# Optimization experiments

Hardware: AMD Instinct MI355X
Metric: run time of the kernel (lower is better)

## Reference

```python
import jax, jax.numpy as jnp
import numpy as np

EPS = 1e-5  # BatchNorm eps (torch default)

def _bn(x, gamma, beta):
    # training-mode BatchNorm over the edge/node (leading) axis, biased var
    mean = x.mean(axis=0, keepdims=True)
    var = x.var(axis=0, keepdims=True)
    return (x - mean) * jax.lax.rsqrt(var + EPS) * gamma + beta

def _silu(x):
    return x * jax.nn.sigmoid(x)

def setup_inputs() -> dict:
    N, E, H, NH = 50000, 800000, 128, 4
    HD = H // NH
    key = jax.random.key(0)
    ks = jax.random.split(key, 8)
    x = jax.random.normal(ks[0], (N, H), dtype=jnp.float32)
    weight = jax.random.uniform(ks[1], (N, 1), dtype=jnp.float32)  # positive fraction weights
    src = jax.random.randint(ks[2], (E,), 0, N)
    dst = jax.random.randint(ks[3], (E,), 0, N)
    # f: Linear(2H, 1) + BN(1)
    Wf = jax.random.normal(ks[4], (2 * H, 1), dtype=jnp.float32) * 0.05
    bf = jnp.zeros((1,), jnp.float32)
    f_gamma = jnp.ones((1,), jnp.float32)
    f_beta = jnp.zeros((1,), jnp.float32)
    # g: NH heads of Linear(2H, HD) + BN(HD), stacked on leading head axis
    Wg = jax.random.normal(ks[5], (NH, 2 * H, HD), dtype=jnp.float32) * 0.05
    bg = jnp.zeros((NH, HD), jnp.float32)
    g_gamma = jnp.ones((NH, HD), jnp.float32)
    g_beta = jnp.zeros((NH, HD), jnp.float32)
    # bn_nodes: BN(H)
    n_gamma = jnp.ones((H,), jnp.float32)
    n_beta = jnp.zeros((H,), jnp.float32)
    return dict(x=x, weight=weight, src=src, dst=dst, Wf=Wf, bf=bf,
                f_gamma=f_gamma, f_beta=f_beta, Wg=Wg, bg=bg,
                g_gamma=g_gamma, g_beta=g_beta, n_gamma=n_gamma, n_beta=n_beta)

def reference(x, weight, src, dst, Wf, bf, f_gamma, f_beta, Wg, bg, g_gamma, g_beta, n_gamma, n_beta):
    N = x.shape[0]
    E = src.shape[0]
    # per-edge concat of src/dst node features: [E, 2H]
    hihj = jnp.concatenate([x[src], x[dst]], axis=-1)
    # attention logit f(hihj) = SiLU(BN(Linear)) then exp: [E, 1]
    exp_e = jnp.exp(_silu(_bn(hihj @ Wf + bf, f_gamma, f_beta)))
    # weighted softmax-like normalization over incoming edges of each dst node
    we = weight[src] * exp_e                                   # [E, 1]
    sum_w_exp = jax.ops.segment_sum(we, dst, num_segments=N)   # [N, 1]
    a = we / sum_w_exp[dst]                                    # [E, 1]
    # multi-head message: a_ij * SiLU(BN(Linear_h(hihj))) per head, concat
    z = jnp.einsum('ed,hdk->ehk', hihj, Wg) + bg               # [E, NH, HD]
    z = _silu(_bn(z, g_gamma, g_beta))
    msg = (a[:, :, None] * z).reshape(E, -1)                   # [E, H]
    h = jax.ops.segment_sum(msg, dst, num_segments=N)          # [N, H]
    out = _bn(h, n_gamma, n_beta) + x                          # residual
    return out
```

## Files before the change

kernel.cpp:

```cpp
#include <hip/hip_runtime.h>
#include <hip/hip_bf16.h>
#include <math.h>

#define HDIM 128
#define PAD 64
#define QCAP 8192
typedef unsigned short ushort_t;
typedef unsigned int uint_t;
typedef __attribute__((ext_vector_type(8))) short bf16x8;
typedef __attribute__((ext_vector_type(4))) float f32x4;
typedef __attribute__((ext_vector_type(2))) float v2f;

__device__ __forceinline__ float wave_allreduce(float v){
  #pragma unroll
  for (int o = 1; o < 64; o <<= 1) v += __shfl_xor(v, o);
  return v;
}

__device__ __forceinline__ ushort_t f2bf(float f){
  uint_t u = __float_as_uint(f);
  uint_t r = (u + 0x7fffu + ((u >> 16) & 1u)) >> 16;
  return (ushort_t)r;
}

__device__ __forceinline__ v2f bf2(uint_t u){
  v2f r;
  r.x = __uint_as_float(u << 16);
  r.y = __uint_as_float(u & 0xffff0000u);
  return r;
}

__global__ __launch_bounds__(256) void k_wpack(const float* __restrict__ Wg,
    const float* __restrict__ Wf, ushort_t* __restrict__ W3,
    const int* __restrict__ src, const int* __restrict__ dst,
    uint_t* __restrict__ queue, int* __restrict__ tails, int E){
  int b = blockIdx.x;
  if (b < 272){
    int k = threadIdx.x;
    if (k >= 128) return;
    float val;
    if (b < 128)       val = Wg[(size_t)(b >> 5) * 8192 + k * 32 + (b & 31)];
    else if (b < 256){ int c2 = b - 128;
                       val = Wg[(size_t)(c2 >> 5) * 8192 + (k + 128) * 32 + (c2 & 31)]; }
    else if (b == 256) val = Wf[k];
    else if (b == 257) val = Wf[128 + k];
    else               val = 0.f;
    int idx = (((b >> 4) * 4 + (k >> 5)) * 16 + (b & 15)) * 32 + (k & 31);
    W3[idx] = f2bf(val);
    return;
  }
  __shared__ int hist[256], gbase[256];
  int t = threadIdx.x;
  hist[t] = 0;
  __syncthreads();
  int e0 = ((b - 272) * 256 + t) * 8;
  int d0=0,d1=0,d2=0,d3=0,d4=0,d5=0,d6=0,d7=0;
  int s0=0,s1=0,s2=0,s3=0,s4=0,s5=0,s6=0,s7=0;
  bool v0=e0<E, v1=e0+1<E, v2=e0+2<E, v3=e0+3<E,
       v4=e0+4<E, v5=e0+5<E, v6=e0+6<E, v7=e0+7<E;
  if (v7 && (e0 + 8 <= E)){
    int4 da = *(const int4*)(dst + e0); int4 db_ = *(const int4*)(dst + e0 + 4);
    int4 sa = *(const int4*)(src + e0); int4 sb_ = *(const int4*)(src + e0 + 4);
    d0=da.x; d1=da.y; d2=da.z; d3=da.w; d4=db_.x; d5=db_.y; d6=db_.z; d7=db_.w;
    s0=sa.x; s1=sa.y; s2=sa.z; s3=sa.w; s4=sb_.x; s5=sb_.y; s6=sb_.z; s7=sb_.w;
  } else {
    if (v0){ d0=dst[e0];   s0=src[e0];   }
    if (v1){ d1=dst[e0+1]; s1=src[e0+1]; }
    if (v2){ d2=dst[e0+2]; s2=src[e0+2]; }
    if (v3){ d3=dst[e0+3]; s3=src[e0+3]; }
    if (v4){ d4=dst[e0+4]; s4=src[e0+4]; }
    if (v5){ d5=dst[e0+5]; s5=src[e0+5]; }
    if (v6){ d6=dst[e0+6]; s6=src[e0+6]; }
    if (v7){ d7=dst[e0+7]; s7=src[e0+7]; }
  }
#define DIST1(i) int b##i = d##i >> 8, r##i = 0; \
    if (v##i) r##i = atomicAdd(&hist[b##i], 1);
  DIST1(0) DIST1(1) DIST1(2) DIST1(3) DIST1(4) DIST1(5) DIST1(6) DIST1(7)
#undef DIST1
  __syncthreads();
  if (hist[t]) gbase[t] = atomicAdd(&tails[t], hist[t]);
  __syncthreads();
#define DISTW(i) if (v##i){ int q = gbase[b##i] + r##i; if (q < QCAP) \
    queue[(size_t)b##i * QCAP + q] = ((uint_t)(d##i & 255) << 16) | (uint_t)s##i; }
  DISTW(0) DISTW(1) DISTW(2) DISTW(3) DISTW(4) DISTW(5) DISTW(6) DISTW(7)
#undef DISTW
}

__global__ __launch_bounds__(256) void k_gemmfill(const float* __restrict__ x,
    const ushort_t* __restrict__ W3, const float* __restrict__ weight,
    ushort_t* __restrict__ Pb, ushort_t* __restrict__ Qb,
    float* __restrict__ v, float2* __restrict__ uw2,
    const uint_t* __restrict__ queue, const int* __restrict__ tails,
    int* __restrict__ cnt, int* __restrict__ es,
    int N, int BK){
  __shared__ ushort_t smem[16384];
  __shared__ int lcnt[256];
  int tid = threadIdx.x;
  if ((int)blockIdx.x < BK){
    int b = blockIdx.x;
    lcnt[tid] = 0;
    __syncthreads();
    int count = tails[b]; if (count > QCAP) count = QCAP;
    for (int i = tid; i < count; i += 256){
      uint_t pk = queue[(size_t)b * QCAP + i];
      int dl = pk >> 16;
      int slot = atomicAdd(&lcnt[dl], 1);
      if (slot < PAD) smem[dl * 64 + slot] = (ushort_t)(pk & 0xffffu);
    }
    __syncthreads();
    int nb = b << 8;
    for (int i = tid; i < 16384; i += 256){
      int n = nb + (i >> 6);
      if (n < N) es[(size_t)nb * 64 + i] = (int)smem[i];
    }
    int n = nb + tid;
    if (n < N){ int c = lcnt[tid]; cnt[n] = c < PAD ? c : PAD; }
  } else {
    ushort_t* xl = smem;
    ushort_t* cl = smem + 4096;
    int n_base = ((int)blockIdx.x - BK) * 32;
    #pragma unroll
    for (int i = 0; i < 4; ++i){
      int cidx = i * 256 + tid;
      int row = cidx >> 5, ch = cidx & 31;
      int rowc = n_base + row; rowc = rowc < N ? rowc : N - 1;
      float4 a = *(const float4*)(x + (size_t)rowc * HDIM + ch * 4);
      uint_t lo = (uint_t)f2bf(a.x) | ((uint_t)f2bf(a.y) << 16);
      uint_t hi = (uint_t)f2bf(a.z) | ((uint_t)f2bf(a.w) << 16);
      int bo = (row * 256 + ch * 8) ^ ((row & 7) << 4);
      *(uint2*)((char*)xl + bo) = make_uint2(lo, hi);
    }
    __syncthreads();
    int wid = __builtin_amdgcn_readfirstlane(tid >> 6);
    int lane = tid & 63;
    int quad = lane >> 4, col = lane & 15;
    int strip = wid >> 1;
    int half = wid & 1;
    int tbeg = half * 8;
    int ntile = half ? 9 : 8;
    f32x4 acc[9];
    #pragma unroll
    for (int t = 0; t < 9; ++t) acc[t] = (f32x4){0.f, 0.f, 0.f, 0.f};
    int arow = strip * 16 + col;
    #pragma unroll
    for (int kk = 0; kk < 4; ++kk){
      int abyte = (arow * 256 + kk * 64 + quad * 16) ^ ((col & 7) << 4);
      bf16x8 af = *(const bf16x8*)((char*)xl + abyte);
      const ushort_t* wb = W3 + (size_t)(tbeg * 4 + kk) * 512 + col * 32 + quad * 8;
      #pragma unroll
      for (int t = 0; t < 9; ++t){
        if (t < ntile){
          bf16x8 bfr = *(const bf16x8*)(wb + (size_t)t * 2048);
          acc[t] = __builtin_amdgcn_mfma_f32_16x16x32_bf16(af, bfr, acc[t], 0, 0, 0);
        }
      }
    }
    #pragma unroll
    for (int t = 0; t < 8; ++t){
      int ct = tbeg + t;
      #pragma unroll
      for (int r = 0; r < 4; ++r){
        int lr = strip * 16 + quad * 4 + r;
        cl[lr * 264 + ct * 16 + col] = f2bf(acc[t][r]);
      }
    }
    if (half){
      #pragma unroll
      for (int r = 0; r < 4; ++r){
        int n = n_base + strip * 16 + quad * 4 + r;
        if (n < N){
          float val = acc[8][r];
          if (col == 0)      uw2[n] = make_float2(val, weight[n]);
          else if (col == 1) v[n] = val;
        }
      }
    }
    __syncthreads();
    int row = tid >> 3, seg = tid & 7;
    int n = n_base + row;
    if (n < N){
      const ushort_t* s = cl + row * 264 + seg * 32;
      uint4 w0 = *(const uint4*)(s);
      uint4 w1 = *(const uint4*)(s + 8);
      uint4 w2 = *(const uint4*)(s + 16);
      uint4 w3v = *(const uint4*)(s + 24);
      if (seg < 4){
        ushort_t* dp = Pb + (size_t)n * HDIM + seg * 32;
        *(uint4*)(dp) = w0; *(uint4*)(dp + 8) = w1;
        *(uint4*)(dp + 16) = w2; *(uint4*)(dp + 24) = w3v;
      } else {
        ushort_t* dp = Qb + (size_t)n * HDIM + (seg - 4) * 32;
        *(uint4*)(dp) = w0; *(uint4*)(dp + 8) = w1;
        *(uint4*)(dp + 16) = w2; *(uint4*)(dp + 24) = w3v;
      }
    }
  }
}

#define SH8(sjv,jj,S) \
  int S##0=__shfl(sjv,(jj)),   S##1=__shfl(sjv,(jj)+1), S##2=__shfl(sjv,(jj)+2), S##3=__shfl(sjv,(jj)+3), \
      S##4=__shfl(sjv,(jj)+4), S##5=__shfl(sjv,(jj)+5), S##6=__shfl(sjv,(jj)+6), S##7=__shfl(sjv,(jj)+7);
#define LD8(S,P) \
  uint_t P##0=Pu[(size_t)S##0*64+lane], P##1=Pu[(size_t)S##1*64+lane], \
         P##2=Pu[(size_t)S##2*64+lane], P##3=Pu[(size_t)S##3*64+lane], \
         P##4=Pu[(size_t)S##4*64+lane], P##5=Pu[(size_t)S##5*64+lane], \
         P##6=Pu[(size_t)S##6*64+lane], P##7=Pu[(size_t)S##7*64+lane];
#define SH4(sjv,jj,S) \
  int S##0=__shfl(sjv,(jj)),   S##1=__shfl(sjv,(jj)+1), S##2=__shfl(sjv,(jj)+2), S##3=__shfl(sjv,(jj)+3);
#define LD4(S,P) \
  uint_t P##0=Pu[(size_t)S##0*64+lane], P##1=Pu[(size_t)S##1*64+lane], \
         P##2=Pu[(size_t)S##2*64+lane], P##3=Pu[(size_t)S##3*64+lane];

__global__ __launch_bounds__(256) void k_gstats(const ushort_t* __restrict__ Pb,
    const ushort_t* __restrict__ Qb, const float* __restrict__ v,
    const float2* __restrict__ uw2, const int* __restrict__ es,
    const int* __restrict__ cnt, float* __restrict__ pstatG, int N){
  int lane = threadIdx.x & 63;
  int wid = __builtin_amdgcn_readfirstlane(threadIdx.x >> 6);
  int part = (int)blockIdx.x & 7;
  int Npp = (N + 7) >> 3;
  int lo = part * Npp;
  int hi = lo + Npp; if (hi > N) hi = N;
  int stp = (gridDim.x >> 3) << 2;
  const uint_t* Pu = (const uint_t*)Pb;
  const uint_t* Qu = (const uint_t*)Qb;
  v2f gs = {0.f,0.f}, gq = {0.f,0.f};
  float fs = 0.f, fq = 0.f;
  int n0 = lo + ((blockIdx.x >> 3) << 2) + wid;
  int n1 = n0 + stp;
  int dnA=0,sjA=0; uint_t qAu=0; float vA=0.f;
  int dnB=0,sjB=0; uint_t qBu=0; float vB=0.f;
  if (n0 < hi){ dnA=cnt[n0]; sjA=es[(size_t)n0*PAD+lane];
                qAu=Qu[(size_t)n0*64+lane]; vA=v[n0]; }
  if (n1 < hi){ dnB=cnt[n1]; sjB=es[(size_t)n1*PAD+lane];
                qBu=Qu[(size_t)n1*64+lane]; vB=v[n1]; }
#define GST(p,Sv,Qv) { v2f y=bf2(p); Sv+=y; Qv.x=fmaf(y.x,y.x,Qv.x); Qv.y=fmaf(y.y,y.y,Qv.y); }
#define GED8(P,Sv,Qv) GST(P##0,Sv,Qv) GST(P##1,Sv,Qv) GST(P##2,Sv,Qv) GST(P##3,Sv,Qv) \
                      GST(P##4,Sv,Qv) GST(P##5,Sv,Qv) GST(P##6,Sv,Qv) GST(P##7,Sv,Qv)
#define GED4(P,Sv,Qv) GST(P##0,Sv,Qv) GST(P##1,Sv,Qv) GST(P##2,Sv,Qv) GST(P##3,Sv,Qv)
  while (n0 < hi){
    int m0 = n0 + 2*stp, m1 = n1 + 2*stp;
    int dnC=0,sjC=0; uint_t qCu=0; float vC=0.f;
    int dnD=0,sjD=0; uint_t qDu=0; float vD=0.f;
    if (m0 < hi){ dnC=cnt[m0]; sjC=es[(size_t)m0*PAD+lane];
                  qCu=Qu[(size_t)m0*64+lane]; vC=v[m0]; }
    if (m1 < hi){ dnD=cnt[m1]; sjD=es[(size_t)m1*PAD+lane];
                  qDu=Qu[(size_t)m1*64+lane]; vD=v[m1]; }
    int dA = dnA < PAD ? dnA : PAD;
    int dB = (n1 < hi) ? (dnB < PAD ? dnB : PAD) : 0;
    if (lane < dA){ float2 uw = uw2[sjA]; float t = uw.x + vA; fs += t; fq = fmaf(t,t,fq); }
    if (lane < dB){ float2 uw = uw2[sjB]; float t = uw.x + vB; fs += t; fq = fmaf(t,t,fq); }
    v2f qa = bf2(qAu), qb = bf2(qBu);
    v2f SnA={0.f,0.f}, SSA={0.f,0.f}, SnB={0.f,0.f}, SSB={0.f,0.f};
    int j0 = 0, j1 = 0;
    for (; j0 + 7 < dA && j1 + 7 < dB; j0 += 8, j1 += 8){
      SH8(sjA,j0,xa) SH8(sjB,j1,xb)
      LD8(xa,pa) LD8(xb,pb)
      GED8(pa,SnA,SSA) GED8(pb,SnB,SSB)
    }
    for (; j0 + 7 < dA; j0 += 8){ SH8(sjA,j0,xa) LD8(xa,pa) GED8(pa,SnA,SSA) }
    for (; j0 + 3 < dA; j0 += 4){ SH4(sjA,j0,xa) LD4(xa,pa) GED4(pa,SnA,SSA) }
    for (; j0 < dA; ++j0){ int s0=__shfl(sjA,j0); uint_t p0=Pu[(size_t)s0*64+lane]; GST(p0,SnA,SSA) }
    for (; j1 + 7 < dB; j1 += 8){ SH8(sjB,j1,xb) LD8(xb,pb) GED8(pb,SnB,SSB) }
    for (; j1 + 3 < dB; j1 += 4){ SH4(sjB,j1,xb) LD4(xb,pb) GED4(pb,SnB,SSB) }
    for (; j1 < dB; ++j1){ int s0=__shfl(sjB,j1); uint_t p0=Pu[(size_t)s0*64+lane]; GST(p0,SnB,SSB) }
    float dAf = (float)dA, dBf = (float)dB;
    gs.x += SnA.x + SnB.x + dAf*qa.x + dBf*qb.x;
    gs.y += SnA.y + SnB.y + dAf*qa.y + dBf*qb.y;
    gq.x += SSA.x + SSB.x + qa.x*fmaf(dAf,qa.x,2.f*SnA.x) + qb.x*fmaf(dBf,qb.x,2.f*SnB.x);
    gq.y += SSA.y + SSB.y + qa.y*fmaf(dAf,qa.y,2.f*SnA.y) + qb.y*fmaf(dBf,qb.y,2.f*SnB.y);
    n0 = m0; n1 = m1;
    dnA=dnC; sjA=sjC; qAu=qCu; vA=vC;
    dnB=dnD; sjB=sjD; qBu=qDu; vB=vD;
  }
#undef GST
#undef GED8
#undef GED4
  fs = wave_allreduce(fs); fq = wave_allreduce(fq);
  __shared__ float red[4][258];
  red[wid][2*lane]       = gs.x; red[wid][2*lane+1]   = gs.y;
  red[wid][128+2*lane]   = gq.x; red[wid][129+2*lane] = gq.y;
  if (lane == 0){ red[wid][256] = fs; red[wid][257] = fq; }
  __syncthreads();
  for (int c = threadIdx.x; c < 258; c += 256)
    pstatG[(size_t)blockIdx.x * 258 + c] = red[0][c] + red[1][c] + red[2][c] + red[3][c];
}

__global__ __launch_bounds__(256) void k_redfin1(const float* __restrict__ pstatG,
    int NB, const float* __restrict__ g_gamma, const float* __restrict__ g_beta,
    const float* __restrict__ f_gamma, const float* __restrict__ f_beta,
    float* __restrict__ fin, long long E){
  int j = blockIdx.x;
  int c1 = (j < 128) ? j : 256;
  int c2 = (j < 128) ? 128 + j : 257;
  double s1 = 0, s2 = 0;
  for (int b = threadIdx.x; b < NB; b += 256){
    const float* pb = pstatG + (size_t)b * 258;
    s1 += (double)pb[c1]; s2 += (double)pb[c2];
  }
  __shared__ double m1[256], m2[256];
  m1[threadIdx.x] = s1; m2[threadIdx.x] = s2;
  __syncthreads();
  for (int o = 128; o; o >>= 1){
    if (threadIdx.x < o){ m1[threadIdx.x] += m1[threadIdx.x + o];
                          m2[threadIdx.x] += m2[threadIdx.x + o]; }
    __syncthreads();
  }
  if (threadIdx.x == 0){
    double m = m1[0] / (double)E;
    double var = m2[0] / (double)E - m * m;
    if (j < 128){
      float sc = (float)((double)g_gamma[j] / sqrt(var + 1e-5));
      fin[2 + j] = sc; fin[130 + j] = g_beta[j] - (float)m * sc;
    } else {
      float sc = (float)((double)f_gamma[0] / sqrt(var + 1e-5));
      fin[0] = sc; fin[1] = f_beta[0] - (float)m * sc;
    }
  }
}

__global__ __launch_bounds__(256) void k_msg(const ushort_t* __restrict__ Pb,
    const ushort_t* __restrict__ Qb, const float* __restrict__ v,
    const float2* __restrict__ uw2, const int* __restrict__ es,
    const int* __restrict__ cnt, const float* __restrict__ fin,
    float* __restrict__ h, float* __restrict__ pstatH, int N){
  int lane = threadIdx.x & 63;
  int wid = __builtin_amdgcn_readfirstlane(threadIdx.x >> 6);
  int part = (int)blockIdx.x & 7;
  int Npp = (N + 7) >> 3;
  int lo = part * Npp;
  int hi = lo + Npp; if (hi > N) hi = N;
  int stp = (gridDim.x >> 3) << 2;
  const uint_t* Pu = (const uint_t*)Pb;
  const uint_t* Qu = (const uint_t*)Qb;
  float fsc = fin[0], fsh = fin[1];
  v2f gsc = {fin[2 + 2*lane], fin[3 + 2*lane]};
  v2f gsh = {fin[130 + 2*lane], fin[131 + 2*lane]};
  v2f hs = {0.f,0.f}, hq = {0.f,0.f};
  int n0 = lo + ((blockIdx.x >> 3) << 2) + wid;
  int n1 = n0 + stp;
  int dnA=0,sjA=0; uint_t qAu=0; float vA=0.f;
  int dnB=0,sjB=0; uint_t qBu=0; float vB=0.f;
  if (n0 < hi){ dnA=cnt[n0]; sjA=es[(size_t)n0*PAD+lane];
                qAu=Qu[(size_t)n0*64+lane]; vA=v[n0]; }
  if (n1 < hi){ dnB=cnt[n1]; sjB=es[(size_t)n1*PAD+lane];
                qBu=Qu[(size_t)n1*64+lane]; vB=v[n1]; }
#define EDGE(p,a,qv,av) { v2f y = (bf2(p) + qv) * gsc + gsh; \
      float e0 = __expf(-y.x), e1 = __expf(-y.y); \
      float d0 = 1.f + e0, d1 = 1.f + e1; \
      float r = __builtin_amdgcn_rcpf(d0 * d1) * (a); \
      av.x = fmaf(y.x * d1, r, av.x); av.y = fmaf(y.y * d0, r, av.y); }
#define ASH8(wjv,jj,A) \
  float A##0=__shfl(wjv,(jj)),   A##1=__shfl(wjv,(jj)+1), A##2=__shfl(wjv,(jj)+2), A##3=__shfl(wjv,(jj)+3), \
        A##4=__shfl(wjv,(jj)+4), A##5=__shfl(wjv,(jj)+5), A##6=__shfl(wjv,(jj)+6), A##7=__shfl(wjv,(jj)+7);
#define ASH4(wjv,jj,A) \
  float A##0=__shfl(wjv,(jj)),   A##1=__shfl(wjv,(jj)+1), A##2=__shfl(wjv,(jj)+2), A##3=__shfl(wjv,(jj)+3);
#define MED8(P,A,qv,av) EDGE(P##0,A##0,qv,av) EDGE(P##1,A##1,qv,av) EDGE(P##2,A##2,qv,av) EDGE(P##3,A##3,qv,av) \
                        EDGE(P##4,A##4,qv,av) EDGE(P##5,A##5,qv,av) EDGE(P##6,A##6,qv,av) EDGE(P##7,A##7,qv,av)
#define MED4(P,A,qv,av) EDGE(P##0,A##0,qv,av) EDGE(P##1,A##1,qv,av) EDGE(P##2,A##2,qv,av) EDGE(P##3,A##3,qv,av)
  while (n0 < hi){
    int m0 = n0 + 2*stp, m1 = n1 + 2*stp;
    int dnC=0,sjC=0; uint_t qCu=0; float vC=0.f;
    int dnD=0,sjD=0; uint_t qDu=0; float vD=0.f;
    if (m0 < hi){ dnC=cnt[m0]; sjC=es[(size_t)m0*PAD+lane];
                  qCu=Qu[(size_t)m0*64+lane]; vC=v[m0]; }
    if (m1 < hi){ dnD=cnt[m1]; sjD=es[(size_t)m1*PAD+lane];
                  qDu=Qu[(size_t)m1*64+lane]; vD=v[m1]; }
    int dA = dnA < PAD ? dnA : PAD;
    int dB = (n1 < hi) ? (dnB < PAD ? dnB : PAD) : 0;
    float wjA = 0.f, wjB = 0.f;
    if (lane < dA){ float2 uw = uw2[sjA];
      float tt = fmaf(uw.x + vA, fsc, fsh);
      float sl = tt * __builtin_amdgcn_rcpf(1.f + __expf(-tt));
      wjA = uw.y * __expf(sl); }
    if (lane < dB){ float2 uw = uw2[sjB];
      float tt = fmaf(uw.x + vB, fsc, fsh);
      float sl = tt * __builtin_amdgcn_rcpf(1.f + __expf(-tt));
      wjB = uw.y * __expf(sl); }
    v2f qa = bf2(qAu), qb = bf2(qBu);
    v2f accA = {0.f,0.f}, accB = {0.f,0.f};
    int j0 = 0, j1 = 0;
    for (; j0 + 7 < dA && j1 + 7 < dB; j0 += 8, j1 += 8){
      SH8(sjA,j0,xa) SH8(sjB,j1,xb)
      ASH8(wjA,j0,aa) ASH8(wjB,j1,ab)
      LD8(xa,pa) LD8(xb,pb)
      MED8(pa,aa,qa,accA) MED8(pb,ab,qb,accB)
    }
    for (; j0 + 7 < dA; j0 += 8){ SH8(sjA,j0,xa) ASH8(wjA,j0,aa) LD8(xa,pa) MED8(pa,aa,qa,accA) }
    for (; j0 + 3 < dA; j0 += 4){ SH4(sjA,j0,xa) ASH4(wjA,j0,aa) LD4(xa,pa) MED4(pa,aa,qa,accA) }
    for (; j0 < dA; ++j0){ int s0=__shfl(sjA,j0); float a0=__shfl(wjA,j0);
                           uint_t p0=Pu[(size_t)s0*64+lane]; EDGE(p0,a0,qa,accA) }
    for (; j1 + 7 < dB; j1 += 8){ SH8(sjB,j1,xb) ASH8(wjB,j1,ab) LD8(xb,pb) MED8(pb,ab,qb,accB) }
    for (; j1 + 3 < dB; j1 += 4){ SH4(sjB,j1,xb) ASH4(wjB,j1,ab) LD4(xb,pb) MED4(pb,ab,qb,accB) }
    for (; j1 < dB; ++j1){ int s0=__shfl(sjB,j1); float a0=__shfl(wjB,j1);
                           uint_t p0=Pu[(size_t)s0*64+lane]; EDGE(p0,a0,qb,accB) }
    float swA = wjA, swB = wjB;
    #pragma unroll
    for (int o = 1; o < 64; o <<= 1){ swA += __shfl_xor(swA, o); swB += __shfl_xor(swB, o); }
    float rsA = (dA > 0) ? (1.f / swA) : 0.f;
    float rsB = (dB > 0) ? (1.f / swB) : 0.f;
    accA.x *= rsA; accA.y *= rsA;
    accB.x *= rsB; accB.y *= rsB;
    *(float2*)&h[(size_t)n0 * 128 + 2*lane] = make_float2(accA.x, accA.y);
    hs += accA; hq += accA * accA;
    if (n1 < hi){
      *(float2*)&h[(size_t)n1 * 128 + 2*lane] = make_float2(accB.x, accB.y);
      hs += accB; hq += accB * accB;
    }
    n0 = m0; n1 = m1;
    dnA=dnC; sjA=sjC; qAu=qCu; vA=vC;
    dnB=dnD; sjB=sjD; qBu=qDu; vB=vD;
  }
#undef EDGE
#undef ASH8
#undef ASH4
#undef MED8
#undef MED4
  __shared__ float red[4][256];
  red[wid][2*lane]       = hs.x; red[wid][2*lane+1]   = hs.y;
  red[wid][128+2*lane]   = hq.x; red[wid][129+2*lane] = hq.y;
  __syncthreads();
  int c = threadIdx.x;
  pstatH[(size_t)blockIdx.x * 256 + c] = red[0][c] + red[1][c] + red[2][c] + red[3][c];
}

__global__ __launch_bounds__(256) void k_redfin2(const float* __restrict__ pstatH,
    int NB, const float* __restrict__ n_gamma, const float* __restrict__ n_beta,
    float* __restrict__ fin, int N){
  int j = blockIdx.x;
  double s1 = 0, s2 = 0;
  for (int b = threadIdx.x; b < NB; b += 256){
    const float* pb = pstatH + (size_t)b * 256;
    s1 += (double)pb[j]; s2 += (double)pb[128 + j];
  }
  __shared__ double m1[256], m2[256];
  m1[threadIdx.x] = s1; m2[threadIdx.x] = s2;
  __syncthreads();
  for (int o = 128; o; o >>= 1){
    if (threadIdx.x < o){ m1[threadIdx.x] += m1[threadIdx.x + o];
                          m2[threadIdx.x] += m2[threadIdx.x + o]; }
    __syncthreads();
  }
  if (threadIdx.x == 0){
    double m = m1[0] / (double)N;
    double var = m2[0] / (double)N - m * m;
    float sc = (float)((double)n_gamma[j] / sqrt(var + 1e-5));
    fin[258 + j] = sc; fin[386 + j] = n_beta[j] - (float)m * sc;
  }
}

__global__ __launch_bounds__(256) void k_out(const float* __restrict__ h,
    const float* __restrict__ x, const float* __restrict__ fin,
    float* __restrict__ out, int total4){
  int i = blockIdx.x * 256 + threadIdx.x;
  if (i >= total4) return;
  const float4* h4 = (const float4*)h; const float4* x4 = (const float4*)x;
  float4 hv = h4[i], xv = x4[i];
  int c = (i * 4) & 127;
  float4 o;
  o.x = fmaf(hv.x, fin[258 + c],     fin[386 + c])     + xv.x;
  o.y = fmaf(hv.y, fin[258 + c + 1], fin[386 + c + 1]) + xv.y;
  o.z = fmaf(hv.z, fin[258 + c + 2], fin[386 + c + 2]) + xv.z;
  o.w = fmaf(hv.w, fin[258 + c + 3], fin[386 + c + 3]) + xv.w;
  ((float4*)out)[i] = o;
}

extern "C" void kernel_launch(void* const* d_in, const int* in_sizes, int n_in,
                              void* d_out, int out_size, void* d_ws, size_t ws_size,
                              hipStream_t stream){
  const float* x       = (const float*)d_in[0];
  const float* weight  = (const float*)d_in[1];
  const int*   src     = (const int*)d_in[2];
  const int*   dst     = (const int*)d_in[3];
  const float* Wf      = (const float*)d_in[4];
  const float* f_gamma = (const float*)d_in[6];
  const float* f_beta  = (const float*)d_in[7];
  const float* Wg      = (const float*)d_in[8];
  const float* g_gamma = (const float*)d_in[10];
  const float* g_beta  = (const float*)d_in[11];
  const float* n_gamma = (const float*)d_in[12];
  const float* n_beta  = (const float*)d_in[13];
  float* out = (float*)d_out;

  int N = in_sizes[0] / HDIM;
  int E = in_sizes[2];

  char* ws = (char*)d_ws;
  size_t off = 0;
  auto alloc = [&](size_t bytes)->char*{
    char* p = ws + off; off = (off + bytes + 255) & ~(size_t)255; return p;
  };
  ushort_t* Pb    = (ushort_t*)alloc((size_t)N * HDIM * 2);
  ushort_t* Qb    = (ushort_t*)alloc((size_t)N * HDIM * 2);
  float* h        = (float*)alloc((size_t)N * HDIM * 4);
  float* v        = (float*)alloc((size_t)N * 4);
  float2* uw2     = (float2*)alloc((size_t)N * 8);
  int* es         = (int*)alloc((size_t)N * PAD * 4);
  ushort_t* W3    = (ushort_t*)alloc((size_t)272 * 128 * 2);
  int* cnt        = (int*)alloc((size_t)N * 4);
  uint_t* queue   = (uint_t*)alloc((size_t)256 * QCAP * 4);
  int* tails      = (int*)alloc(256 * 4);
  const int NWB = 2048;
  const int NB  = NWB;
  float*  pstatG = (float*)alloc((size_t)NB * 258 * 4);
  float*  pstatH = (float*)alloc((size_t)NB * 256 * 4);
  float*  fin    = (float*)alloc(514 * 4);

  int GB = (N + 31) / 32;
  int BK = (N + 255) >> 8;
  int DB = (E + 2047) / 2048;

  hipMemsetAsync(tails, 0, 256 * 4, stream);
  k_wpack   <<<272 + DB, 256, 0, stream>>>(Wg, Wf, W3, src, dst, queue, tails, E);
  k_gemmfill<<<BK + GB, 256, 0, stream>>>(x, W3, weight, Pb, Qb, v, uw2,
                                          queue, tails, cnt, es, N, BK);
  k_gstats  <<<NWB, 256, 0, stream>>>(Pb, Qb, v, uw2, es, cnt, pstatG, N);
  k_redfin1 <<<129, 256, 0, stream>>>(pstatG, NB, g_gamma, g_beta, f_gamma, f_beta, fin, (long long)E);
  k_msg     <<<NWB, 256, 0, stream>>>(Pb, Qb, v, uw2, es, cnt, fin, h, pstatH, N);
  k_redfin2 <<<128, 256, 0, stream>>>(pstatH, NB, n_gamma, n_beta, fin, N);
  k_out     <<<(N * HDIM / 4 + 255) / 256, 256, 0, stream>>>(h, x, fin, out, N * HDIM / 4);
}
```

Baseline: 256.2 us.

## Fuse stats, reductions, message and output into one cooperative grid-synced kernel

```diff
diff --git a/kernel.cpp b/kernel.cpp
--- a/kernel.cpp
+++ b/kernel.cpp
@@ -1,6 +1,9 @@
 #include <hip/hip_runtime.h>
 #include <hip/hip_bf16.h>
+#include <hip/hip_cooperative_groups.h>
 #include <math.h>
+
+namespace cg = cooperative_groups;
 
 #define HDIM 128
 #define PAD 64
@@ -78,7 +81,7 @@
   DIST1(0) DIST1(1) DIST1(2) DIST1(3) DIST1(4) DIST1(5) DIST1(6) DIST1(7)
 #undef DIST1
   __syncthreads();
-  if (hist[t]) gbase[t] = atomicAdd(&tails[t], hist[t]);
+  if (hist[t]) gbase[t] = atomicAdd(&tails[t * 16], hist[t]);
   __syncthreads();
 #define DISTW(i) if (v##i){ int q = gbase[b##i] + r##i; if (q < QCAP) \
     queue[(size_t)b##i * QCAP + q] = ((uint_t)(d##i & 255) << 16) | (uint_t)s##i; }
@@ -100,7 +103,7 @@
     int b = blockIdx.x;
     lcnt[tid] = 0;
     __syncthreads();
-    int count = tails[b]; if (count > QCAP) count = QCAP;
+    int count = tails[b * 16]; if (count > QCAP) count = QCAP;
     for (int i = tid; i < count; i += 256){
       uint_t pk = queue[(size_t)b * QCAP + i];
       int dl = pk >> 16;
@@ -210,11 +213,29 @@
 #define LD4(S,P) \
   uint_t P##0=Pu[(size_t)S##0*64+lane], P##1=Pu[(size_t)S##1*64+lane], \
          P##2=Pu[(size_t)S##2*64+lane], P##3=Pu[(size_t)S##3*64+lane];
-
-__global__ __launch_bounds__(256) void k_gstats(const ushort_t* __restrict__ Pb,
+#define GST(p,Sv,Qv) { v2f y=bf2(p); Sv+=y; Qv.x=fmaf(y.x,y.x,Qv.x); Qv.y=fmaf(y.y,y.y,Qv.y); }
+#define GED8(P,Sv,Qv) GST(P##0,Sv,Qv) GST(P##1,Sv,Qv) GST(P##2,Sv,Qv) GST(P##3,Sv,Qv) \
+                      GST(P##4,Sv,Qv) GST(P##5,Sv,Qv) GST(P##6,Sv,Qv) GST(P##7,Sv,Qv)
+#define GED4(P,Sv,Qv) GST(P##0,Sv,Qv) GST(P##1,Sv,Qv) GST(P##2,Sv,Qv) GST(P##3,Sv,Qv)
+#define EDGE(p,a,qv,av) { v2f y = (bf2(p) + qv) * gsc + gsh; \
+      float e0 = __expf(-y.x), e1 = __expf(-y.y); \
+      float d0 = 1.f + e0, d1 = 1.f + e1; \
+      float r = __builtin_amdgcn_rcpf(d0 * d1) * (a); \
+      av.x = fmaf(y.x * d1, r, av.x); av.y = fmaf(y.y * d0, r, av.y); }
+#define ASH8(wjv,jj,A) \
+  float A##0=__shfl(wjv,(jj)),   A##1=__shfl(wjv,(jj)+1), A##2=__shfl(wjv,(jj)+2), A##3=__shfl(wjv,(jj)+3), \
+        A##4=__shfl(wjv,(jj)+4), A##5=__shfl(wjv,(jj)+5), A##6=__shfl(wjv,(jj)+6), A##7=__shfl(wjv,(jj)+7);
+#define ASH4(wjv,jj,A) \
+  float A##0=__shfl(wjv,(jj)),   A##1=__shfl(wjv,(jj)+1), A##2=__shfl(wjv,(jj)+2), A##3=__shfl(wjv,(jj)+3);
+#define MED8(P,A,qv,av) EDGE(P##0,A##0,qv,av) EDGE(P##1,A##1,qv,av) EDGE(P##2,A##2,qv,av) EDGE(P##3,A##3,qv,av) \
+                        EDGE(P##4,A##4,qv,av) EDGE(P##5,A##5,qv,av) EDGE(P##6,A##6,qv,av) EDGE(P##7,A##7,qv,av)
+#define MED4(P,A,qv,av) EDGE(P##0,A##0,qv,av) EDGE(P##1,A##1,qv,av) EDGE(P##2,A##2,qv,av) EDGE(P##3,A##3,qv,av)
+
+__device__ __forceinline__ void gstats_body(const ushort_t* __restrict__ Pb,
     const ushort_t* __restrict__ Qb, const float* __restrict__ v,
     const float2* __restrict__ uw2, const int* __restrict__ es,
-    const int* __restrict__ cnt, float* __restrict__ pstatG, int N){
+    const int* __restrict__ cnt, float* __restrict__ pstatG, int N,
+    float (*red)[258]){
   int lane = threadIdx.x & 63;
   int wid = __builtin_amdgcn_readfirstlane(threadIdx.x >> 6);
   int part = (int)blockIdx.x & 7;
@@ -234,10 +255,6 @@
                 qAu=Qu[(size_t)n0*64+lane]; vA=v[n0]; }
   if (n1 < hi){ dnB=cnt[n1]; sjB=es[(size_t)n1*PAD+lane];
                 qBu=Qu[(size_t)n1*64+lane]; vB=v[n1]; }
-#define GST(p,Sv,Qv) { v2f y=bf2(p); Sv+=y; Qv.x=fmaf(y.x,y.x,Qv.x); Qv.y=fmaf(y.y,y.y,Qv.y); }
-#define GED8(P,Sv,Qv) GST(P##0,Sv,Qv) GST(P##1,Sv,Qv) GST(P##2,Sv,Qv) GST(P##3,Sv,Qv) \
-                      GST(P##4,Sv,Qv) GST(P##5,Sv,Qv) GST(P##6,Sv,Qv) GST(P##7,Sv,Qv)
-#define GED4(P,Sv,Qv) GST(P##0,Sv,Qv) GST(P##1,Sv,Qv) GST(P##2,Sv,Qv) GST(P##3,Sv,Qv)
   while (n0 < hi){
     int m0 = n0 + 2*stp, m1 = n1 + 2*stp;
     int dnC=0,sjC=0; uint_t qCu=0; float vC=0.f;
@@ -273,11 +290,7 @@
     dnA=dnC; sjA=sjC; qAu=qCu; vA=vC;
     dnB=dnD; sjB=sjD; qBu=qDu; vB=vD;
   }
-#undef GST
-#undef GED8
-#undef GED4
   fs = wave_allreduce(fs); fq = wave_allreduce(fq);
-  __shared__ float red[4][258];
   red[wid][2*lane]       = gs.x; red[wid][2*lane+1]   = gs.y;
   red[wid][128+2*lane]   = gq.x; red[wid][129+2*lane] = gq.y;
   if (lane == 0){ red[wid][256] = fs; red[wid][257] = fq; }
@@ -286,11 +299,10 @@
     pstatG[(size_t)blockIdx.x * 258 + c] = red[0][c] + red[1][c] + red[2][c] + red[3][c];
 }
 
-__global__ __launch_bounds__(256) void k_redfin1(const float* __restrict__ pstatG,
+__device__ __forceinline__ void redfin1_body(const float* __restrict__ pstatG,
     int NB, const float* __restrict__ g_gamma, const float* __restrict__ g_beta,
     const float* __restrict__ f_gamma, const float* __restrict__ f_beta,
-    float* __restrict__ fin, long long E){
-  int j = blockIdx.x;
+    float* __restrict__ fin, long long E, int j, double* m1, double* m2){
   int c1 = (j < 128) ? j : 256;
   int c2 = (j < 128) ? 128 + j : 257;
   double s1 = 0, s2 = 0;
@@ -298,7 +310,6 @@
     const float* pb = pstatG + (size_t)b * 258;
     s1 += (double)pb[c1]; s2 += (double)pb[c2];
   }
-  __shared__ double m1[256], m2[256];
   m1[threadIdx.x] = s1; m2[threadIdx.x] = s2;
   __syncthreads();
   for (int o = 128; o; o >>= 1){
@@ -319,11 +330,12 @@
   }
 }
 
-__global__ __launch_bounds__(256) void k_msg(const ushort_t* __restrict__ Pb,
+__device__ __forceinline__ void msg_body(const ushort_t* __restrict__ Pb,
     const ushort_t* __restrict__ Qb, const float* __restrict__ v,
     const float2* __restrict__ uw2, const int* __restrict__ es,
     const int* __restrict__ cnt, const float* __restrict__ fin,
-    float* __restrict__ h, float* __restrict__ pstatH, int N){
+    float* __restrict__ h, float* __restrict__ pstatH, int N,
+    float (*red)[258]){
   int lane = threadIdx.x & 63;
   int wid = __builtin_amdgcn_readfirstlane(threadIdx.x >> 6);
   int part = (int)blockIdx.x & 7;
@@ -345,19 +357,6 @@
                 qAu=Qu[(size_t)n0*64+lane]; vA=v[n0]; }
   if (n1 < hi){ dnB=cnt[n1]; sjB=es[(size_t)n1*PAD+lane];
                 qBu=Qu[(size_t)n1*64+lane]; vB=v[n1]; }
-#define EDGE(p,a,qv,av) { v2f y = (bf2(p) + qv) * gsc + gsh; \
-      float e0 = __expf(-y.x), e1 = __expf(-y.y); \
-      float d0 = 1.f + e0, d1 = 1.f + e1; \
-      float r = __builtin_amdgcn_rcpf(d0 * d1) * (a); \
-      av.x = fmaf(y.x * d1, r, av.x); av.y = fmaf(y.y * d0, r, av.y); }
-#define ASH8(wjv,jj,A) \
-  float A##0=__shfl(wjv,(jj)),   A##1=__shfl(wjv,(jj)+1), A##2=__shfl(wjv,(jj)+2), A##3=__shfl(wjv,(jj)+3), \
-        A##4=__shfl(wjv,(jj)+4), A##5=__shfl(wjv,(jj)+5), A##6=__shfl(wjv,(jj)+6), A##7=__shfl(wjv,(jj)+7);
-#define ASH4(wjv,jj,A) \
-  float A##0=__shfl(wjv,(jj)),   A##1=__shfl(wjv,(jj)+1), A##2=__shfl(wjv,(jj)+2), A##3=__shfl(wjv,(jj)+3);
-#define MED8(P,A,qv,av) EDGE(P##0,A##0,qv,av) EDGE(P##1,A##1,qv,av) EDGE(P##2,A##2,qv,av) EDGE(P##3,A##3,qv,av) \
-                        EDGE(P##4,A##4,qv,av) EDGE(P##5,A##5,qv,av) EDGE(P##6,A##6,qv,av) EDGE(P##7,A##7,qv,av)
-#define MED4(P,A,qv,av) EDGE(P##0,A##0,qv,av) EDGE(P##1,A##1,qv,av) EDGE(P##2,A##2,qv,av) EDGE(P##3,A##3,qv,av)
   while (n0 < hi){
     int m0 = n0 + 2*stp, m1 = n1 + 2*stp;
     int dnC=0,sjC=0; uint_t qCu=0; float vC=0.f;
@@ -411,12 +410,6 @@
     dnA=dnC; sjA=sjC; qAu=qCu; vA=vC;
     dnB=dnD; sjB=sjD; qBu=qDu; vB=vD;
   }
-#undef EDGE
-#undef ASH8
-#undef ASH4
-#undef MED8
-#undef MED4
-  __shared__ float red[4][256];
   red[wid][2*lane]       = hs.x; red[wid][2*lane+1]   = hs.y;
   red[wid][128+2*lane]   = hq.x; red[wid][129+2*lane] = hq.y;
   __syncthreads();
@@ -424,16 +417,14 @@
   pstatH[(size_t)blockIdx.x * 256 + c] = red[0][c] + red[1][c] + red[2][c] + red[3][c];
 }
 
-__global__ __launch_bounds__(256) void k_redfin2(const float* __restrict__ pstatH,
+__device__ __forceinline__ void redfin2_body(const float* __restrict__ pstatH,
     int NB, const float* __restrict__ n_gamma, const float* __restrict__ n_beta,
-    float* __restrict__ fin, int N){
-  int j = blockIdx.x;
+    float* __restrict__ fin, int N, int j, double* m1, double* m2){
   double s1 = 0, s2 = 0;
   for (int b = threadIdx.x; b < NB; b += 256){
     const float* pb = pstatH + (size_t)b * 256;
     s1 += (double)pb[j]; s2 += (double)pb[128 + j];
   }
-  __shared__ double m1[256], m2[256];
   m1[threadIdx.x] = s1; m2[threadIdx.x] = s2;
   __syncthreads();
   for (int o = 128; o; o >>= 1){
@@ -449,20 +440,83 @@
   }
 }
 
+__device__ __forceinline__ void out_body(const float* __restrict__ h,
+    const float* __restrict__ x, const float* __restrict__ fin,
+    float* __restrict__ out, int total4){
+  const float4* h4 = (const float4*)h; const float4* x4 = (const float4*)x;
+  for (int i = blockIdx.x * 256 + threadIdx.x; i < total4; i += gridDim.x * 256){
+    float4 hv = h4[i], xv = x4[i];
+    int c = (i * 4) & 127;
+    float4 o;
+    o.x = fmaf(hv.x, fin[258 + c],     fin[386 + c])     + xv.x;
+    o.y = fmaf(hv.y, fin[258 + c + 1], fin[386 + c + 1]) + xv.y;
+    o.z = fmaf(hv.z, fin[258 + c + 2], fin[386 + c + 2]) + xv.z;
+    o.w = fmaf(hv.w, fin[258 + c + 3], fin[386 + c + 3]) + xv.w;
+    ((float4*)out)[i] = o;
+  }
+}
+
+__global__ __launch_bounds__(256) void k_gstats(const ushort_t* __restrict__ Pb,
+    const ushort_t* __restrict__ Qb, const float* __restrict__ v,
+    const float2* __restrict__ uw2, const int* __restrict__ es,
+    const int* __restrict__ cnt, float* __restrict__ pstatG, int N){
+  __shared__ float red[4][258];
+  gstats_body(Pb, Qb, v, uw2, es, cnt, pstatG, N, red);
+}
+
+__global__ __launch_bounds__(256) void k_redfin1(const float* __restrict__ pstatG,
+    int NB, const float* __restrict__ g_gamma, const float* __restrict__ g_beta,
+    const float* __restrict__ f_gamma, const float* __restrict__ f_beta,
+    float* __restrict__ fin, long long E){
+  __shared__ double m1[256], m2[256];
+  redfin1_body(pstatG, NB, g_gamma, g_beta, f_gamma, f_beta, fin, E, blockIdx.x, m1, m2);
+}
+
+__global__ __launch_bounds__(256) void k_msg(const ushort_t* __restrict__ Pb,
+    const ushort_t* __restrict__ Qb, const float* __restrict__ v,
+    const float2* __restrict__ uw2, const int* __restrict__ es,
+    const int* __restrict__ cnt, const float* __restrict__ fin,
+    float* __restrict__ h, float* __restrict__ pstatH, int N){
+  __shared__ float red[4][258];
+  msg_body(Pb, Qb, v, uw2, es, cnt, fin, h, pstatH, N, red);
+}
+
+__global__ __launch_bounds__(256) void k_redfin2(const float* __restrict__ pstatH,
+    int NB, const float* __restrict__ n_gamma, const float* __restrict__ n_beta,
+    float* __restrict__ fin, int N){
+  __shared__ double m1[256], m2[256];
+  redfin2_body(pstatH, NB, n_gamma, n_beta, fin, N, blockIdx.x, m1, m2);
+}
+
 __global__ __launch_bounds__(256) void k_out(const float* __restrict__ h,
     const float* __restrict__ x, const float* __restrict__ fin,
     float* __restrict__ out, int total4){
-  int i = blockIdx.x * 256 + threadIdx.x;
-  if (i >= total4) return;
-  const float4* h4 = (const float4*)h; const float4* x4 = (const float4*)x;
-  float4 hv = h4[i], xv = x4[i];
-  int c = (i * 4) & 127;
-  float4 o;
-  o.x = fmaf(hv.x, fin[258 + c],     fin[386 + c])     + xv.x;
-  o.y = fmaf(hv.y, fin[258 + c + 1], fin[386 + c + 1]) + xv.y;
-  o.z = fmaf(hv.z, fin[258 + c + 2], fin[386 + c + 2]) + xv.z;
-  o.w = fmaf(hv.w, fin[258 + c + 3], fin[386 + c + 3]) + xv.w;
-  ((float4*)out)[i] = o;
+  out_body(h, x, fin, out, total4);
+}
+
+__global__ __launch_bounds__(256) void k_fused(const ushort_t* Pb,
+    const ushort_t* Qb, const float* v, const float2* uw2, const int* es,
+    const int* cnt, float* fin, float* h, const float* x, float* out,
+    float* pstatG, float* pstatH,
+    const float* g_gamma, const float* g_beta,
+    const float* f_gamma, const float* f_beta,
+    const float* n_gamma, const float* n_beta,
+    int N, long long E, int total4){
+  cg::grid_group grid = cg::this_grid();
+  __shared__ float red[4][258];
+  __shared__ double m1[256], m2[256];
+  gstats_body(Pb, Qb, v, uw2, es, cnt, pstatG, N, red);
+  grid.sync();
+  if (blockIdx.x < 129)
+    redfin1_body(pstatG, gridDim.x, g_gamma, g_beta, f_gamma, f_beta, fin, E,
+                 blockIdx.x, m1, m2);
+  grid.sync();
+  msg_body(Pb, Qb, v, uw2, es, cnt, fin, h, pstatH, N, red);
+  grid.sync();
+  if (blockIdx.x < 128)
+    redfin2_body(pstatH, gridDim.x, n_gamma, n_beta, fin, N, blockIdx.x, m1, m2);
+  grid.sync();
+  out_body(h, x, fin, out, total4);
 }
 
 extern "C" void kernel_launch(void* const* d_in, const int* in_sizes, int n_in,
@@ -499,24 +553,54 @@
   ushort_t* W3    = (ushort_t*)alloc((size_t)272 * 128 * 2);
   int* cnt        = (int*)alloc((size_t)N * 4);
   uint_t* queue   = (uint_t*)alloc((size_t)256 * QCAP * 4);
-  int* tails      = (int*)alloc(256 * 4);
-  const int NWB = 2048;
-  const int NB  = NWB;
-  float*  pstatG = (float*)alloc((size_t)NB * 258 * 4);
-  float*  pstatH = (float*)alloc((size_t)NB * 256 * 4);
-  float*  fin    = (float*)alloc(514 * 4);
+  int* tails      = (int*)alloc((size_t)256 * 16 * 4);
+  float*  pstatG  = (float*)alloc((size_t)2048 * 258 * 4);
+  float*  pstatH  = (float*)alloc((size_t)2048 * 256 * 4);
+  float*  fin     = (float*)alloc(514 * 4);
 
   int GB = (N + 31) / 32;
   int BK = (N + 255) >> 8;
   int DB = (E + 2047) / 2048;
-
-  hipMemsetAsync(tails, 0, 256 * 4, stream);
+  long long Ell = E;
+  int total4 = N * HDIM / 4;
+
+  static int coopBlocks = -2;
+  if (coopBlocks == -2){
+    int nb = 0;
+    if (hipOccupancyMaxActiveBlocksPerMultiprocessor(&nb,
+          (const void*)k_fused, 256, 0) != hipSuccess) nb = 0;
+    coopBlocks = nb;
+  }
+  int G = 0;
+  if (coopBlocks > 0){
+    long long g = (long long)coopBlocks * 256;
+    if (g > 2048) g = 2048;
+    G = (int)(g & ~7LL);
+    if (G < 8) G = 8;
+  }
+
+  hipMemsetAsync(tails, 0, (size_t)256 * 16 * 4, stream);
   k_wpack   <<<272 + DB, 256, 0, stream>>>(Wg, Wf, W3, src, dst, queue, tails, E);
   k_gemmfill<<<BK + GB, 256, 0, stream>>>(x, W3, weight, Pb, Qb, v, uw2,
                                           queue, tails, cnt, es, N, BK);
-  k_gstats  <<<NWB, 256, 0, stream>>>(Pb, Qb, v, uw2, es, cnt, pstatG, N);
-  k_redfin1 <<<129, 256, 0, stream>>>(pstatG, NB, g_gamma, g_beta, f_gamma, f_beta, fin, (long long)E);
-  k_msg     <<<NWB, 256, 0, stream>>>(Pb, Qb, v, uw2, es, cnt, fin, h, pstatH, N);
-  k_redfin2 <<<128, 256, 0, stream>>>(pstatH, NB, n_gamma, n_beta, fin, N);
-  k_out     <<<(N * HDIM / 4 + 255) / 256, 256, 0, stream>>>(h, x, fin, out, N * HDIM / 4);
-}
+  bool fused_ok = false;
+  if (G > 0){
+    void* kargs[] = { (void*)&Pb, (void*)&Qb, (void*)&v, (void*)&uw2, (void*)&es,
+                      (void*)&cnt, (void*)&fin, (void*)&h, (void*)&x, (void*)&out,
+                      (void*)&pstatG, (void*)&pstatH,
+                      (void*)&g_gamma, (void*)&g_beta, (void*)&f_gamma,
+                      (void*)&f_beta, (void*)&n_gamma, (void*)&n_beta,
+                      (void*)&N, (void*)&Ell, (void*)&total4 };
+    hipError_t err = hipLaunchCooperativeKernel((const void*)k_fused,
+                        dim3(G), dim3(256), kargs, 0, stream);
+    fused_ok = (err == hipSuccess);
+  }
+  if (!fused_ok){
+    const int NWB = 2048;
+    k_gstats  <<<NWB, 256, 0, stream>>>(Pb, Qb, v, uw2, es, cnt, pstatG, N);
+    k_redfin1 <<<129, 256, 0, stream>>>(pstatG, NWB, g_gamma, g_beta, f_gamma, f_beta, fin, Ell);
+    k_msg     <<<NWB, 256, 0, stream>>>(Pb, Qb, v, uw2, es, cnt, fin, h, pstatH, N);
+    k_redfin2 <<<128, 256, 0, stream>>>(pstatH, NWB, n_gamma, n_beta, fin, N);
+    k_out     <<<(total4 + 255) / 256, 256, 0, stream>>>(h, x, fin, out, total4);
+  }
+}
```

New measurement: 531.0 us. 2.07x slower.
